# Kernel tuning notes

Measured on AMD Instinct MI355X. Metric: run time of the kernel, lower is better.

Reference implementation:

```python
import jax, jax.numpy as jnp
import numpy as np
import math

B, L, D, H = 2, 2048, 1024, 16
HD = D // H

def setup_inputs() -> dict:
    key = jax.random.key(0)
    ks = jax.random.split(key, 8)
    s = 1.0 / math.sqrt(D)
    # causal additive mask: 0 on/below diagonal, -inf above
    causal = jnp.where(jnp.tril(jnp.ones((L, L), dtype=bool)), 0.0, -jnp.inf)
    causal = causal[None, None].astype(jnp.float32)  # [1,1,L,L]
    return {
        "Q": jax.random.normal(ks[0], (B, L, D), jnp.float32),
        "K": jax.random.normal(ks[1], (B, L, D), jnp.float32),
        "V": jax.random.normal(ks[2], (B, L, D), jnp.float32),
        "attn_mask": causal,
        "padding_mask": jnp.zeros((B, L), dtype=bool),
        "wq": jax.random.normal(ks[3], (D, D), jnp.float32) * s,
        "wk": jax.random.normal(ks[4], (D, D), jnp.float32) * s,
        "wv": jax.random.normal(ks[5], (D, D), jnp.float32) * s,
        "wout": jax.random.normal(ks[6], (D, D), jnp.float32) * s,
    }

def reference(Q, K, V, attn_mask, padding_mask, wq, wk, wv, wout):
    b, l, _ = Q.shape
    # projections (torch Linear: x @ W.T); weights sampled as [out,in]-like square
    def proj(x, w):
        return (x @ w.T).reshape(b, l, H, HD).transpose(0, 2, 1, 3)  # [B,H,L,hd]
    q = proj(Q, wq)
    k = proj(K, wk)
    v = proj(V, wv)
    scores = jnp.einsum("bhqd,bhkd->bhqk", q, k) / math.sqrt(HD)
    scores = scores + attn_mask
    scores = jnp.where(padding_mask[:, None, None, :], -jnp.inf, scores)
    weights = jax.nn.softmax(scores, axis=-1)
    ctx = jnp.einsum("bhqk,bhkd->bhqd", weights, v)
    ctx = ctx.transpose(0, 2, 1, 3).reshape(b, l, D)
    return ctx @ wout.T
```

## Files before the change

kernel.cpp:

```cpp
#include <hip/hip_runtime.h>
#include <stdint.h>
#include <stddef.h>

typedef __bf16 bf16_t;
typedef bf16_t bf16x4 __attribute__((ext_vector_type(4)));
typedef bf16_t bf16x8 __attribute__((ext_vector_type(8)));
typedef float f32x4 __attribute__((ext_vector_type(4)));

#define MFMA_BF16(A_, B_, C_) __builtin_amdgcn_mfma_f32_16x16x32_bf16(A_, B_, C_, 0, 0, 0)

static constexpr int Lseq = 2048;
static constexpr int Dmod = 1024;
static constexpr int Hn   = 16;
static constexpr int HDim = 64;
static constexpr size_t M1 = 1u << 20;

__device__ __forceinline__ int swz(int row, int chunk) {
  return row * 64 + ((chunk ^ (row & 7)) << 3);
}

__device__ __forceinline__ void async_ld16(const bf16_t* g, bf16_t* l) {
  __builtin_amdgcn_global_load_lds(
      (const __attribute__((address_space(1))) void*)g,
      (__attribute__((address_space(3))) void*)l, 16, 0, 0);
}

__global__ __launch_bounds__(256) void cvt_kernel(
    const float* __restrict__ Q, const float* __restrict__ K,
    const float* __restrict__ V, const float* __restrict__ wq,
    const float* __restrict__ wk, const float* __restrict__ wv,
    const float* __restrict__ wout, bf16_t* __restrict__ wsb)
{
  const int s = blockIdx.z;
  const float* __restrict__ src;
  if      (s < 4)   src = Q    + (size_t)s * M1;
  else if (s < 8)   src = K    + (size_t)(s - 4) * M1;
  else if (s < 12)  src = V    + (size_t)(s - 8) * M1;
  else if (s == 12) src = wq;
  else if (s == 13) src = wk;
  else if (s == 14) src = wv;
  else              src = wout;
  bf16_t* __restrict__ dst = wsb + (size_t)s * M1;
  const float scale = (s == 12) ? 0.18033688f : 1.0f;

  const int idx = blockIdx.x * 256 + threadIdx.x;
  float4 a = ((const float4*)src)[idx * 2];
  float4 b = ((const float4*)src)[idx * 2 + 1];
  bf16x8 o;
  o[0] = (bf16_t)(a.x * scale); o[1] = (bf16_t)(a.y * scale);
  o[2] = (bf16_t)(a.z * scale); o[3] = (bf16_t)(a.w * scale);
  o[4] = (bf16_t)(b.x * scale); o[5] = (bf16_t)(b.y * scale);
  o[6] = (bf16_t)(b.z * scale); o[7] = (bf16_t)(b.w * scale);
  ((bf16x8*)dst)[idx] = o;
}

__global__ __launch_bounds__(256) void proj_kernel(
    const bf16_t* __restrict__ Qbf, const bf16_t* __restrict__ Kbf,
    const bf16_t* __restrict__ Vbf, const bf16_t* __restrict__ wqb,
    const bf16_t* __restrict__ wkb, const bf16_t* __restrict__ wvb,
    bf16_t* __restrict__ qo, bf16_t* __restrict__ ko, bf16_t* __restrict__ vo)
{
  const int z = blockIdx.z;
  const bf16_t* __restrict__ A  = (z == 0) ? Qbf : (z == 1) ? Kbf : Vbf;
  const bf16_t* __restrict__ Bw = (z == 0) ? wqb : (z == 1) ? wkb : wvb;
  bf16_t* __restrict__ dst      = (z == 0) ? qo  : (z == 1) ? ko  : vo;

  __shared__ __align__(16) bf16_t As[128 * 64];
  __shared__ __align__(16) bf16_t Bs[64 * 64];

  const int tid  = threadIdx.x;
  const int wave = tid >> 6;
  const int lane = tid & 63;
  const int quad = lane >> 4;
  const int l16  = lane & 15;
  const int wm   = (wave & 1) * 64;
  const int wn   = (wave >> 1) * 32;
  const int m0   = blockIdx.x * 128;
  const int n0   = blockIdx.y * 64;

  const int srow8  = lane >> 3;
  const int schunk = (lane & 7) ^ srow8;

  f32x4 acc[4][2];
#pragma unroll
  for (int i = 0; i < 4; ++i)
#pragma unroll
    for (int j = 0; j < 2; ++j)
#pragma unroll
      for (int e = 0; e < 4; ++e) acc[i][j][e] = 0.0f;

  for (int kt = 0; kt < 16; ++kt) {
    const int k0 = kt * 64;
    __syncthreads();
#pragma unroll
    for (int i = 0; i < 4; ++i) {
      const int rb = wave * 32 + i * 8;
      async_ld16(&A[(size_t)(m0 + rb + srow8) * Dmod + k0 + schunk * 8], &As[rb * 64]);
    }
#pragma unroll
    for (int i = 0; i < 2; ++i) {
      const int rb = wave * 16 + i * 8;
      async_ld16(&Bw[(size_t)(n0 + rb + srow8) * Dmod + k0 + schunk * 8], &Bs[rb * 64]);
    }
    __syncthreads();

    bf16x8 af[4][2], bfr[2][2];
#pragma unroll
    for (int mt = 0; mt < 4; ++mt) {
      const int row = wm + mt * 16 + l16;
      af[mt][0] = *(const bf16x8*)&As[swz(row, quad)];
      af[mt][1] = *(const bf16x8*)&As[swz(row, quad + 4)];
    }
#pragma unroll
    for (int nt = 0; nt < 2; ++nt) {
      const int row = wn + nt * 16 + l16;
      bfr[nt][0] = *(const bf16x8*)&Bs[swz(row, quad)];
      bfr[nt][1] = *(const bf16x8*)&Bs[swz(row, quad + 4)];
    }
#pragma unroll
    for (int mt = 0; mt < 4; ++mt)
#pragma unroll
      for (int nt = 0; nt < 2; ++nt) {
        acc[mt][nt] = MFMA_BF16(af[mt][0], bfr[nt][0], acc[mt][nt]);
        acc[mt][nt] = MFMA_BF16(af[mt][1], bfr[nt][1], acc[mt][nt]);
      }
  }

#pragma unroll
  for (int mt = 0; mt < 4; ++mt) {
    const int grb = m0 + wm + mt * 16 + quad * 4;
    const int bb  = grb >> 11;
    const int lb  = grb & 2047;
#pragma unroll
    for (int nt = 0; nt < 2; ++nt) {
      const int gc = n0 + wn + nt * 16 + l16;
      const int h  = gc >> 6;
      const int hd = gc & 63;
      if (z == 2) {
        bf16x4 pk;
#pragma unroll
        for (int r = 0; r < 4; ++r) pk[r] = (bf16_t)acc[mt][nt][r];
        *(bf16x4*)&dst[(((size_t)(bb * Hn + h) * HDim + hd) << 11) + lb] = pk;
      } else {
#pragma unroll
        for (int r = 0; r < 4; ++r)
          dst[(((size_t)(bb * Hn + h) * Lseq + lb + r) << 6) + hd] = (bf16_t)acc[mt][nt][r];
      }
    }
  }
}

__global__ __launch_bounds__(256) void attn_kernel(
    const bf16_t* __restrict__ q, const bf16_t* __restrict__ k,
    const bf16_t* __restrict__ v, bf16_t* __restrict__ ctx)
{
  const int bh = blockIdx.x;
  const int qt = 31 - blockIdx.y;
  const int bb = bh >> 4;
  const int h  = bh & 15;
  const int q0 = qt * 64;

  const int tid  = threadIdx.x;
  const int wave = tid >> 6;
  const int lane = tid & 63;
  const int quad = lane >> 4;
  const int l16  = lane & 15;

  __shared__ __align__(16) bf16_t Ks[64 * 64];
  __shared__ __align__(16) bf16_t Vs[64 * 64];
  __shared__ __align__(16) bf16_t Ps[4][16][72];

  const bf16_t* __restrict__ qb = q + (size_t)bh * (Lseq * HDim);
  const bf16_t* __restrict__ kb = k + (size_t)bh * (Lseq * HDim);
  const bf16_t* __restrict__ vb = v + (size_t)bh * (HDim * Lseq);

  const int srow8  = lane >> 3;
  const int schunk = (lane & 7) ^ srow8;

  bf16x8 ones;
#pragma unroll
  for (int i = 0; i < 8; ++i) ones[i] = (bf16_t)1.0f;

  const int qrow = q0 + wave * 16 + l16;
  bf16x8 qf0 = *(const bf16x8*)&qb[(size_t)qrow * HDim + quad * 8];
  bf16x8 qf1 = *(const bf16x8*)&qb[(size_t)qrow * HDim + 32 + quad * 8];

  f32x4 o[4];
  f32x4 lacc;
#pragma unroll
  for (int e = 0; e < 4; ++e) lacc[e] = 0.0f;
#pragma unroll
  for (int nt = 0; nt < 4; ++nt)
#pragma unroll
    for (int e = 0; e < 4; ++e) o[nt][e] = 0.0f;

  for (int jt = 0; jt <= qt; ++jt) {
    const int j0 = jt * 64;
    __syncthreads();
#pragma unroll
    for (int i = 0; i < 2; ++i) {
      const int rb = wave * 16 + i * 8;
      const int r  = rb + srow8;
      async_ld16(&kb[(size_t)(j0 + r) * HDim + schunk * 8], &Ks[rb * 64]);
      async_ld16(&vb[(size_t)r * Lseq + j0 + schunk * 8], &Vs[rb * 64]);
    }
    __syncthreads();

    f32x4 s[4];
#pragma unroll
    for (int nt = 0; nt < 4; ++nt) {
#pragma unroll
      for (int e = 0; e < 4; ++e) s[nt][e] = 0.0f;
      const int krow = nt * 16 + l16;
      bf16x8 kf0 = *(const bf16x8*)&Ks[swz(krow, quad)];
      bf16x8 kf1 = *(const bf16x8*)&Ks[swz(krow, quad + 4)];
      s[nt] = MFMA_BF16(kf0, qf0, s[nt]);
      s[nt] = MFMA_BF16(kf1, qf1, s[nt]);
    }

    const bool diag = (jt == qt);
#pragma unroll
    for (int nt = 0; nt < 4; ++nt) {
      bf16x4 pk;
#pragma unroll
      for (int r = 0; r < 4; ++r) {
        float val = s[nt][r];
        if (diag && (nt * 16 + quad * 4 + r > wave * 16 + l16)) val = -1e30f;
        pk[r] = (bf16_t)__builtin_amdgcn_exp2f(val);
      }
      *(bf16x4*)&Ps[wave][l16][nt * 16 + quad * 4] = pk;
    }

    bf16x8 pf0 = *(const bf16x8*)&Ps[wave][l16][quad * 8];
    bf16x8 pf1 = *(const bf16x8*)&Ps[wave][l16][32 + quad * 8];

    lacc = MFMA_BF16(pf0, ones, lacc);
    lacc = MFMA_BF16(pf1, ones, lacc);

#pragma unroll
    for (int nt = 0; nt < 4; ++nt) {
      const int vrow = nt * 16 + l16;
      bf16x8 vf0 = *(const bf16x8*)&Vs[swz(vrow, quad)];
      bf16x8 vf1 = *(const bf16x8*)&Vs[swz(vrow, quad + 4)];
      o[nt] = MFMA_BF16(pf0, vf0, o[nt]);
      o[nt] = MFMA_BF16(pf1, vf1, o[nt]);
    }
  }

  float inv[4];
#pragma unroll
  for (int r = 0; r < 4; ++r) inv[r] = 1.0f / lacc[r];
#pragma unroll
  for (int nt = 0; nt < 4; ++nt)
#pragma unroll
    for (int r = 0; r < 4; ++r) {
      const int gq = q0 + wave * 16 + quad * 4 + r;
      ctx[(size_t)(bb * Lseq + gq) * Dmod + h * HDim + nt * 16 + l16] =
          (bf16_t)(o[nt][r] * inv[r]);
    }
}

__global__ __launch_bounds__(256) void out_kernel(
    const bf16_t* __restrict__ Actx, const bf16_t* __restrict__ Bwout,
    float* __restrict__ out)
{
  __shared__ __align__(16) bf16_t As[128 * 64];
  __shared__ __align__(16) bf16_t Bs[64 * 64];

  const int tid  = threadIdx.x;
  const int wave = tid >> 6;
  const int lane = tid & 63;
  const int quad = lane >> 4;
  const int l16  = lane & 15;
  const int wm   = (wave & 1) * 64;
  const int wn   = (wave >> 1) * 32;
  const int m0   = blockIdx.x * 128;
  const int n0   = blockIdx.y * 64;

  const int srow8  = lane >> 3;
  const int schunk = (lane & 7) ^ srow8;

  f32x4 acc[4][2];
#pragma unroll
  for (int i = 0; i < 4; ++i)
#pragma unroll
    for (int j = 0; j < 2; ++j)
#pragma unroll
      for (int e = 0; e < 4; ++e) acc[i][j][e] = 0.0f;

  for (int kt = 0; kt < 16; ++kt) {
    const int k0 = kt * 64;
    __syncthreads();
#pragma unroll
    for (int i = 0; i < 4; ++i) {
      const int rb = wave * 32 + i * 8;
      async_ld16(&Actx[(size_t)(m0 + rb + srow8) * Dmod + k0 + schunk * 8], &As[rb * 64]);
    }
#pragma unroll
    for (int i = 0; i < 2; ++i) {
      const int rb = wave * 16 + i * 8;
      async_ld16(&Bwout[(size_t)(n0 + rb + srow8) * Dmod + k0 + schunk * 8], &Bs[rb * 64]);
    }
    __syncthreads();

    bf16x8 af[4][2], bfr[2][2];
#pragma unroll
    for (int mt = 0; mt < 4; ++mt) {
      const int row = wm + mt * 16 + l16;
      af[mt][0] = *(const bf16x8*)&As[swz(row, quad)];
      af[mt][1] = *(const bf16x8*)&As[swz(row, quad + 4)];
    }
#pragma unroll
    for (int nt = 0; nt < 2; ++nt) {
      const int row = wn + nt * 16 + l16;
      bfr[nt][0] = *(const bf16x8*)&Bs[swz(row, quad)];
      bfr[nt][1] = *(const bf16x8*)&Bs[swz(row, quad + 4)];
    }
#pragma unroll
    for (int mt = 0; mt < 4; ++mt)
#pragma unroll
      for (int nt = 0; nt < 2; ++nt) {
        acc[mt][nt] = MFMA_BF16(af[mt][0], bfr[nt][0], acc[mt][nt]);
        acc[mt][nt] = MFMA_BF16(af[mt][1], bfr[nt][1], acc[mt][nt]);
      }
  }

#pragma unroll
  for (int mt = 0; mt < 4; ++mt) {
    const int grb = m0 + wm + mt * 16 + quad * 4;
#pragma unroll
    for (int nt = 0; nt < 2; ++nt) {
      const int gc = n0 + wn + nt * 16 + l16;
#pragma unroll
      for (int r = 0; r < 4; ++r)
        out[(size_t)(grb + r) * Dmod + gc] = acc[mt][nt][r];
    }
  }
}

extern "C" void kernel_launch(void* const* d_in, const int* in_sizes, int n_in,
                              void* d_out, int out_size, void* d_ws, size_t ws_size,
                              hipStream_t stream) {
  (void)in_sizes; (void)n_in; (void)out_size; (void)ws_size;
  const float* Q    = (const float*)d_in[0];
  const float* K    = (const float*)d_in[1];
  const float* V    = (const float*)d_in[2];
  const float* wq   = (const float*)d_in[5];
  const float* wk   = (const float*)d_in[6];
  const float* wv   = (const float*)d_in[7];
  const float* wout = (const float*)d_in[8];
  float* out = (float*)d_out;

  bf16_t* wsb = (bf16_t*)d_ws;
  bf16_t* Qbf   = wsb;
  bf16_t* Kbf   = wsb + 4 * M1;
  bf16_t* Vbf   = wsb + 8 * M1;
  bf16_t* wqb   = wsb + 12 * M1;
  bf16_t* wkb   = wsb + 13 * M1;
  bf16_t* wvb   = wsb + 14 * M1;
  bf16_t* woutb = wsb + 15 * M1;
  bf16_t* qp    = wsb + 16 * M1;
  bf16_t* kp    = wsb + 20 * M1;
  bf16_t* vp    = wsb + 24 * M1;
  bf16_t* cws   = wsb;

  cvt_kernel<<<dim3(512, 1, 16), 256, 0, stream>>>(Q, K, V, wq, wk, wv, wout, wsb);
  proj_kernel<<<dim3(32, 16, 3), 256, 0, stream>>>(Qbf, Kbf, Vbf, wqb, wkb, wvb, qp, kp, vp);
  attn_kernel<<<dim3(32, 32), 256, 0, stream>>>(qp, kp, vp, cws);
  out_kernel<<<dim3(32, 16), 256, 0, stream>>>(cws, woutb, out);
}
```

Before: 212.6 us.

## Give each attention wave two 16-row query tiles to reuse K/V fragments

```diff
diff --git a/kernel.cpp b/kernel.cpp
--- a/kernel.cpp
+++ b/kernel.cpp
@@ -150,7 +150,7 @@
   }
 }
 
-__global__ __launch_bounds__(256) void attn_kernel(
+__global__ __launch_bounds__(128) void attn_kernel(
     const bf16_t* __restrict__ q, const bf16_t* __restrict__ k,
     const bf16_t* __restrict__ v, bf16_t* __restrict__ ctx)
 {
@@ -168,7 +168,7 @@
 
   __shared__ __align__(16) bf16_t Ks[64 * 64];
   __shared__ __align__(16) bf16_t Vs[64 * 64];
-  __shared__ __align__(16) bf16_t Ps[4][16][72];
+  __shared__ __align__(16) bf16_t Ps[2][32][72];
 
   const bf16_t* __restrict__ qb = q + (size_t)bh * (Lseq * HDim);
   const bf16_t* __restrict__ kb = k + (size_t)bh * (Lseq * HDim);
@@ -181,83 +181,104 @@
 #pragma unroll
   for (int i = 0; i < 8; ++i) ones[i] = (bf16_t)1.0f;
 
-  const int qrow = q0 + wave * 16 + l16;
-  bf16x8 qf0 = *(const bf16x8*)&qb[(size_t)qrow * HDim + quad * 8];
-  bf16x8 qf1 = *(const bf16x8*)&qb[(size_t)qrow * HDim + 32 + quad * 8];
-
-  f32x4 o[4];
-  f32x4 lacc;
-#pragma unroll
-  for (int e = 0; e < 4; ++e) lacc[e] = 0.0f;
-#pragma unroll
-  for (int nt = 0; nt < 4; ++nt)
-#pragma unroll
-    for (int e = 0; e < 4; ++e) o[nt][e] = 0.0f;
+  bf16x8 qf[2][2];
+#pragma unroll
+  for (int mt = 0; mt < 2; ++mt) {
+    const int qrow = q0 + wave * 32 + mt * 16 + l16;
+    qf[mt][0] = *(const bf16x8*)&qb[(size_t)qrow * HDim + quad * 8];
+    qf[mt][1] = *(const bf16x8*)&qb[(size_t)qrow * HDim + 32 + quad * 8];
+  }
+
+  f32x4 o[2][4];
+  f32x4 lacc[2];
+#pragma unroll
+  for (int mt = 0; mt < 2; ++mt) {
+#pragma unroll
+    for (int e = 0; e < 4; ++e) lacc[mt][e] = 0.0f;
+#pragma unroll
+    for (int nt = 0; nt < 4; ++nt)
+#pragma unroll
+      for (int e = 0; e < 4; ++e) o[mt][nt][e] = 0.0f;
+  }
 
   for (int jt = 0; jt <= qt; ++jt) {
     const int j0 = jt * 64;
     __syncthreads();
 #pragma unroll
-    for (int i = 0; i < 2; ++i) {
-      const int rb = wave * 16 + i * 8;
+    for (int i = 0; i < 4; ++i) {
+      const int rb = wave * 32 + i * 8;
       const int r  = rb + srow8;
       async_ld16(&kb[(size_t)(j0 + r) * HDim + schunk * 8], &Ks[rb * 64]);
       async_ld16(&vb[(size_t)r * Lseq + j0 + schunk * 8], &Vs[rb * 64]);
     }
     __syncthreads();
 
-    f32x4 s[4];
+    f32x4 s[2][4];
 #pragma unroll
     for (int nt = 0; nt < 4; ++nt) {
-#pragma unroll
-      for (int e = 0; e < 4; ++e) s[nt][e] = 0.0f;
       const int krow = nt * 16 + l16;
       bf16x8 kf0 = *(const bf16x8*)&Ks[swz(krow, quad)];
       bf16x8 kf1 = *(const bf16x8*)&Ks[swz(krow, quad + 4)];
-      s[nt] = MFMA_BF16(kf0, qf0, s[nt]);
-      s[nt] = MFMA_BF16(kf1, qf1, s[nt]);
+#pragma unroll
+      for (int mt = 0; mt < 2; ++mt) {
+#pragma unroll
+        for (int e = 0; e < 4; ++e) s[mt][nt][e] = 0.0f;
+        s[mt][nt] = MFMA_BF16(kf0, qf[mt][0], s[mt][nt]);
+        s[mt][nt] = MFMA_BF16(kf1, qf[mt][1], s[mt][nt]);
+      }
     }
 
     const bool diag = (jt == qt);
 #pragma unroll
-    for (int nt = 0; nt < 4; ++nt) {
-      bf16x4 pk;
-#pragma unroll
-      for (int r = 0; r < 4; ++r) {
-        float val = s[nt][r];
-        if (diag && (nt * 16 + quad * 4 + r > wave * 16 + l16)) val = -1e30f;
-        pk[r] = (bf16_t)__builtin_amdgcn_exp2f(val);
-      }
-      *(bf16x4*)&Ps[wave][l16][nt * 16 + quad * 4] = pk;
-    }
-
-    bf16x8 pf0 = *(const bf16x8*)&Ps[wave][l16][quad * 8];
-    bf16x8 pf1 = *(const bf16x8*)&Ps[wave][l16][32 + quad * 8];
-
-    lacc = MFMA_BF16(pf0, ones, lacc);
-    lacc = MFMA_BF16(pf1, ones, lacc);
+    for (int mt = 0; mt < 2; ++mt)
+#pragma unroll
+      for (int nt = 0; nt < 4; ++nt) {
+        bf16x4 pk;
+#pragma unroll
+        for (int r = 0; r < 4; ++r) {
+          float val = s[mt][nt][r];
+          if (diag && (nt * 16 + quad * 4 + r > wave * 32 + mt * 16 + l16)) val = -1e30f;
+          pk[r] = (bf16_t)__builtin_amdgcn_exp2f(val);
+        }
+        *(bf16x4*)&Ps[wave][mt * 16 + l16][nt * 16 + quad * 4] = pk;
+      }
+
+    bf16x8 pf[2][2];
+#pragma unroll
+    for (int mt = 0; mt < 2; ++mt) {
+      pf[mt][0] = *(const bf16x8*)&Ps[wave][mt * 16 + l16][quad * 8];
+      pf[mt][1] = *(const bf16x8*)&Ps[wave][mt * 16 + l16][32 + quad * 8];
+      lacc[mt] = MFMA_BF16(pf[mt][0], ones, lacc[mt]);
+      lacc[mt] = MFMA_BF16(pf[mt][1], ones, lacc[mt]);
+    }
 
 #pragma unroll
     for (int nt = 0; nt < 4; ++nt) {
       const int vrow = nt * 16 + l16;
       bf16x8 vf0 = *(const bf16x8*)&Vs[swz(vrow, quad)];
       bf16x8 vf1 = *(const bf16x8*)&Vs[swz(vrow, quad + 4)];
-      o[nt] = MFMA_BF16(pf0, vf0, o[nt]);
-      o[nt] = MFMA_BF16(pf1, vf1, o[nt]);
-    }
-  }
-
-  float inv[4];
-#pragma unroll
-  for (int r = 0; r < 4; ++r) inv[r] = 1.0f / lacc[r];
-#pragma unroll
-  for (int nt = 0; nt < 4; ++nt)
-#pragma unroll
-    for (int r = 0; r < 4; ++r) {
-      const int gq = q0 + wave * 16 + quad * 4 + r;
-      ctx[(size_t)(bb * Lseq + gq) * Dmod + h * HDim + nt * 16 + l16] =
-          (bf16_t)(o[nt][r] * inv[r]);
-    }
+#pragma unroll
+      for (int mt = 0; mt < 2; ++mt) {
+        o[mt][nt] = MFMA_BF16(pf[mt][0], vf0, o[mt][nt]);
+        o[mt][nt] = MFMA_BF16(pf[mt][1], vf1, o[mt][nt]);
+      }
+    }
+  }
+
+#pragma unroll
+  for (int mt = 0; mt < 2; ++mt) {
+    float inv[4];
+#pragma unroll
+    for (int r = 0; r < 4; ++r) inv[r] = 1.0f / lacc[mt][r];
+#pragma unroll
+    for (int nt = 0; nt < 4; ++nt)
+#pragma unroll
+      for (int r = 0; r < 4; ++r) {
+        const int gq = q0 + wave * 32 + mt * 16 + quad * 4 + r;
+        ctx[(size_t)(bb * Lseq + gq) * Dmod + h * HDim + nt * 16 + l16] =
+            (bf16_t)(o[mt][nt][r] * inv[r]);
+      }
+  }
 }
 
 __global__ __launch_bounds__(256) void out_kernel(
@@ -366,6 +387,6 @@
 
   cvt_kernel<<<dim3(512, 1, 16), 256, 0, stream>>>(Q, K, V, wq, wk, wv, wout, wsb);
   proj_kernel<<<dim3(32, 16, 3), 256, 0, stream>>>(Qbf, Kbf, Vbf, wqb, wkb, wvb, qp, kp, vp);
-  attn_kernel<<<dim3(32, 32), 256, 0, stream>>>(qp, kp, vp, cws);
+  attn_kernel<<<dim3(32, 32), 128, 0, stream>>>(qp, kp, vp, cws);
   out_kernel<<<dim3(32, 16), 256, 0, stream>>>(cws, woutb, out);
 }
```

After: 220.1 us. 3.6% more time.

## Load K/V fragments directly from global memory instead of staging through LDS

Applied to the files above, without the earlier changes.

```diff
diff --git a/kernel.cpp b/kernel.cpp
--- a/kernel.cpp
+++ b/kernel.cpp
@@ -166,17 +166,12 @@
   const int quad = lane >> 4;
   const int l16  = lane & 15;
 
-  __shared__ __align__(16) bf16_t Ks[64 * 64];
-  __shared__ __align__(16) bf16_t Vs[64 * 64];
   __shared__ __align__(16) bf16_t Ps[4][16][72];
 
   const bf16_t* __restrict__ qb = q + (size_t)bh * (Lseq * HDim);
   const bf16_t* __restrict__ kb = k + (size_t)bh * (Lseq * HDim);
   const bf16_t* __restrict__ vb = v + (size_t)bh * (HDim * Lseq);
 
-  const int srow8  = lane >> 3;
-  const int schunk = (lane & 7) ^ srow8;
-
   bf16x8 ones;
 #pragma unroll
   for (int i = 0; i < 8; ++i) ones[i] = (bf16_t)1.0f;
@@ -185,6 +180,9 @@
   bf16x8 qf0 = *(const bf16x8*)&qb[(size_t)qrow * HDim + quad * 8];
   bf16x8 qf1 = *(const bf16x8*)&qb[(size_t)qrow * HDim + 32 + quad * 8];
 
+  const bf16_t* __restrict__ krow0 = kb + (size_t)l16 * HDim + quad * 8;
+  const bf16_t* __restrict__ vrow0 = vb + (size_t)l16 * Lseq + quad * 8;
+
   f32x4 o[4];
   f32x4 lacc;
 #pragma unroll
@@ -196,26 +194,30 @@
 
   for (int jt = 0; jt <= qt; ++jt) {
     const int j0 = jt * 64;
-    __syncthreads();
-#pragma unroll
-    for (int i = 0; i < 2; ++i) {
-      const int rb = wave * 16 + i * 8;
-      const int r  = rb + srow8;
-      async_ld16(&kb[(size_t)(j0 + r) * HDim + schunk * 8], &Ks[rb * 64]);
-      async_ld16(&vb[(size_t)r * Lseq + j0 + schunk * 8], &Vs[rb * 64]);
-    }
-    __syncthreads();
+
+    bf16x8 kf[4][2];
+#pragma unroll
+    for (int nt = 0; nt < 4; ++nt) {
+      const bf16_t* kr = krow0 + (size_t)(j0 + nt * 16) * HDim;
+      kf[nt][0] = *(const bf16x8*)kr;
+      kf[nt][1] = *(const bf16x8*)(kr + 32);
+    }
 
     f32x4 s[4];
 #pragma unroll
     for (int nt = 0; nt < 4; ++nt) {
 #pragma unroll
       for (int e = 0; e < 4; ++e) s[nt][e] = 0.0f;
-      const int krow = nt * 16 + l16;
-      bf16x8 kf0 = *(const bf16x8*)&Ks[swz(krow, quad)];
-      bf16x8 kf1 = *(const bf16x8*)&Ks[swz(krow, quad + 4)];
-      s[nt] = MFMA_BF16(kf0, qf0, s[nt]);
-      s[nt] = MFMA_BF16(kf1, qf1, s[nt]);
+      s[nt] = MFMA_BF16(kf[nt][0], qf0, s[nt]);
+      s[nt] = MFMA_BF16(kf[nt][1], qf1, s[nt]);
+    }
+
+    bf16x8 vf[4][2];
+#pragma unroll
+    for (int nt = 0; nt < 4; ++nt) {
+      const bf16_t* vr = vrow0 + (size_t)nt * 16 * Lseq + j0;
+      vf[nt][0] = *(const bf16x8*)vr;
+      vf[nt][1] = *(const bf16x8*)(vr + 32);
     }
 
     const bool diag = (jt == qt);
@@ -239,11 +241,8 @@
 
 #pragma unroll
     for (int nt = 0; nt < 4; ++nt) {
-      const int vrow = nt * 16 + l16;
-      bf16x8 vf0 = *(const bf16x8*)&Vs[swz(vrow, quad)];
-      bf16x8 vf1 = *(const bf16x8*)&Vs[swz(vrow, quad + 4)];
-      o[nt] = MFMA_BF16(pf0, vf0, o[nt]);
-      o[nt] = MFMA_BF16(pf1, vf1, o[nt]);
+      o[nt] = MFMA_BF16(pf0, vf[nt][0], o[nt]);
+      o[nt] = MFMA_BF16(pf1, vf[nt][1], o[nt]);
     }
   }
 
```

Result: slower. 318.2 us (+49.7%).
